# Kernel optimization log

Measured on AMD Instinct MI355X. Metric: run time of the kernel, lower is better.

Reference implementation:

```python
import jax, jax.numpy as jnp
import numpy as np

DIM = 1024
LATENT = 512
HEADS = 16
HEAD_DIM = DIM // HEADS


def setup_inputs() -> dict:
    key = jax.random.key(0)
    ks = jax.random.split(key, 9)
    s = 0.02
    return {
        "x": jax.random.normal(ks[0], (2, 2048, DIM), dtype=jnp.float32),
        "Wq": jax.random.normal(ks[1], (DIM, DIM), dtype=jnp.float32) * s,
        "Wkv": jax.random.normal(ks[2], (DIM, 2 * DIM), dtype=jnp.float32) * s,
        "Wk1": jax.random.normal(ks[3], (DIM, LATENT), dtype=jnp.float32) * s,
        "Wk2": jax.random.normal(ks[4], (LATENT, DIM), dtype=jnp.float32) * s,
        "Wv1": jax.random.normal(ks[5], (DIM, LATENT), dtype=jnp.float32) * s,
        "Wv2": jax.random.normal(ks[6], (LATENT, DIM), dtype=jnp.float32) * s,
        "Wo": jax.random.normal(ks[7], (DIM, DIM), dtype=jnp.float32) * s,
        "bo": jax.random.normal(ks[8], (DIM,), dtype=jnp.float32) * s,
    }


def reference(x, Wq, Wkv, Wk1, Wk2, Wv1, Wv2, Wo, bo):
    b, n, dim = x.shape
    scale = HEAD_DIM ** -0.5
    q = x @ Wq                               # [b, n, dim]
    kv = x @ Wkv                             # [b, n, 2*dim]
    k, v = kv[..., :dim], kv[..., dim:]
    # latent bottleneck MLPs (Linear -> ReLU -> Linear, no bias)
    k = jax.nn.relu(k @ Wk1) @ Wk2           # [b, n, dim]
    v = jax.nn.relu(v @ Wv1) @ Wv2           # [b, n, dim]
    # split heads: [b, n, h*d] -> [b, h, n, d]
    def split_heads(t):
        return t.reshape(b, n, HEADS, HEAD_DIM).transpose(0, 2, 1, 3)
    q = split_heads(q) * scale
    k = split_heads(k)
    v = split_heads(v)
    scores = jnp.einsum('bhid,bhjd->bhij', q, k)   # [b, h, n, n]
    attn = jax.nn.softmax(scores, axis=-1)
    out = jnp.einsum('bhij,bhjd->bhid', attn, v)   # [b, h, n, d]
    out = out.transpose(0, 2, 1, 3).reshape(b, n, dim)
    return out @ Wo + bo
```

## Files before the change

### kernel.cpp

```cpp
#include <hip/hip_runtime.h>
#include <stdint.h>


typedef __attribute__((ext_vector_type(8))) __bf16 bf16x8;
typedef __attribute__((ext_vector_type(4))) float f32x4;

__device__ inline unsigned short f2bfu(float f) {
    __bf16 b = (__bf16)f;
    return __builtin_bit_cast(unsigned short, b);
}

__device__ inline float exp2_fast(float f) {
    return __builtin_amdgcn_exp2f(f);
}

__device__ inline void load_lds16(const void* g, void* l) {
    __builtin_amdgcn_global_load_lds(
        (const __attribute__((address_space(1))) uint32_t*)g,
        (__attribute__((address_space(3))) uint32_t*)l, 16, 0, 0);
}

__device__ inline f32x4 mfma_bf16(bf16x8 a, bf16x8 b, f32x4 c) {
    return __builtin_amdgcn_mfma_f32_16x16x32_bf16(a, b, c, 0, 0, 0);
}


__global__ __launch_bounds__(256) void cvt_x_kernel(
    const float* __restrict__ src, unsigned short* __restrict__ dst)
{
    int i = (blockIdx.x * 256 + threadIdx.x) * 4;
    float4 v = *(const float4*)&src[i];
    ushort4 o;
    o.x = f2bfu(v.x); o.y = f2bfu(v.y); o.z = f2bfu(v.z); o.w = f2bfu(v.w);
    *(ushort4*)&dst[i] = o;
}

__global__ __launch_bounds__(256) void transpose_w2_kernel(
    const float* __restrict__ s0, const float* __restrict__ s1,
    unsigned short* __restrict__ d0, unsigned short* __restrict__ d1,
    int R, int C, float sc0, float sc1)
{
    const float* src = blockIdx.z ? s1 : s0;
    unsigned short* dst = blockIdx.z ? d1 : d0;
    float sc = blockIdx.z ? sc1 : sc0;
    __shared__ float tile[64][65];
    int c0 = blockIdx.x * 64, r0 = blockIdx.y * 64;
    int t = threadIdx.x;
    int col = t & 63, rr = t >> 6;
#pragma unroll
    for (int i = 0; i < 16; ++i)
        tile[rr + i * 4][col] = src[(size_t)(r0 + rr + i * 4) * C + c0 + col];
    __syncthreads();
#pragma unroll
    for (int i = 0; i < 16; ++i) {
        int r2 = rr + i * 4;
        dst[(size_t)(c0 + r2) * R + r0 + col] = f2bfu(tile[col][r2] * sc);
    }
}

__global__ __launch_bounds__(256) void transpose_v_kernel(
    const unsigned short* __restrict__ v, int ldv, unsigned short* __restrict__ vt)
{
    __shared__ unsigned short tile[64][65];
    int n0 = blockIdx.x * 64, bh = blockIdx.y;
    int b = bh >> 4, h = bh & 15;
    int t = threadIdx.x;
    int r = t >> 3, c = t & 7;
#pragma unroll
    for (int p = 0; p < 2; ++p) {
        int row = r + p * 32;
        const unsigned short* src = v + (size_t)(b * 2048 + n0 + row) * ldv + h * 64 + c * 8;
        ushort4 a = *(const ushort4*)src;
        ushort4 b4 = *(const ushort4*)(src + 4);
        tile[row][c * 8 + 0] = a.x;  tile[row][c * 8 + 1] = a.y;
        tile[row][c * 8 + 2] = a.z;  tile[row][c * 8 + 3] = a.w;
        tile[row][c * 8 + 4] = b4.x; tile[row][c * 8 + 5] = b4.y;
        tile[row][c * 8 + 6] = b4.z; tile[row][c * 8 + 7] = b4.w;
    }
    __syncthreads();
#pragma unroll
    for (int p = 0; p < 2; ++p) {
        int d = r + p * 32;
        ushort4 o0, o1;
        o0.x = tile[c * 8 + 0][d]; o0.y = tile[c * 8 + 1][d];
        o0.z = tile[c * 8 + 2][d]; o0.w = tile[c * 8 + 3][d];
        o1.x = tile[c * 8 + 4][d]; o1.y = tile[c * 8 + 5][d];
        o1.z = tile[c * 8 + 6][d]; o1.w = tile[c * 8 + 7][d];
        unsigned short* dp = vt + (size_t)(bh * 64 + d) * 2048 + n0 + c * 8;
        *(ushort4*)dp = o0;
        *(ushort4*)(dp + 4) = o1;
    }
}

template<int BN>
__global__ __launch_bounds__(256) void gemm_bf16_kernel(
    const unsigned short* __restrict__ A0, const unsigned short* __restrict__ A1,
    const unsigned short* __restrict__ B0, const unsigned short* __restrict__ B1,
    void* __restrict__ C0, void* __restrict__ C1,
    int lda, int ldb, int ldc, int K,
    const float* __restrict__ bias, int relu, int out_f32)
{
    const unsigned short* A = blockIdx.z ? A1 : A0;
    const unsigned short* Bt = blockIdx.z ? B1 : B0;
    void* C = blockIdx.z ? C1 : C0;

    constexpr int NI = BN / 32;
    __shared__ unsigned short Als[128 * 32];
    __shared__ unsigned short Bls[BN * 32];
    int t = threadIdx.x;
    int lane = t & 63, w = t >> 6;
    int n0 = blockIdx.x * BN, m0 = blockIdx.y * 128;
    int wm = (w & 1) * 64, wn = (w >> 1) * (BN / 2);
    int lrow = lane & 15, quad = lane >> 4;

    f32x4 acc[4][NI];
    f32x4 z = {0.f, 0.f, 0.f, 0.f};
#pragma unroll
    for (int i = 0; i < 4; ++i)
#pragma unroll
        for (int j = 0; j < NI; ++j) acc[i][j] = z;

    int c0 = t, c1 = t + 256;
    const unsigned short* ag0 = A + (size_t)(m0 + (c0 >> 2)) * lda + (c0 & 3) * 8;
    const unsigned short* ag1 = A + (size_t)(m0 + (c1 >> 2)) * lda + (c1 & 3) * 8;
    const unsigned short* bg0 = Bt + (size_t)(n0 + (c0 >> 2)) * ldb + (c0 & 3) * 8;
    const unsigned short* bg1 = Bt + (size_t)(n0 + ((c1 >> 2) & (BN - 1))) * ldb + (c1 & 3) * 8;

    for (int k0 = 0; k0 < K; k0 += 32) {
        __syncthreads();
        load_lds16(ag0 + k0, &Als[c0 * 8]);
        load_lds16(ag1 + k0, &Als[c1 * 8]);
        load_lds16(bg0 + k0, &Bls[c0 * 8]);
        if constexpr (BN == 128) load_lds16(bg1 + k0, &Bls[c1 * 8]);
        __syncthreads();

        bf16x8 af[4], bfr[NI];
#pragma unroll
        for (int mi = 0; mi < 4; ++mi)
            af[mi] = *(const bf16x8*)&Als[(wm + mi * 16 + lrow) * 32 + quad * 8];
#pragma unroll
        for (int ni = 0; ni < NI; ++ni)
            bfr[ni] = *(const bf16x8*)&Bls[(wn + ni * 16 + lrow) * 32 + quad * 8];
#pragma unroll
        for (int mi = 0; mi < 4; ++mi)
#pragma unroll
            for (int ni = 0; ni < NI; ++ni)
                acc[mi][ni] = mfma_bf16(af[mi], bfr[ni], acc[mi][ni]);
    }

#pragma unroll
    for (int mi = 0; mi < 4; ++mi)
#pragma unroll
        for (int ni = 0; ni < NI; ++ni)
#pragma unroll
            for (int r = 0; r < 4; ++r) {
                int row = m0 + wm + mi * 16 + quad * 4 + r;
                int col = n0 + wn + ni * 16 + lrow;
                float v = acc[mi][ni][r];
                if (bias) v += bias[col];
                if (relu) v = fmaxf(v, 0.0f);
                if (out_f32) ((float*)C)[(size_t)row * ldc + col] = v;
                else ((unsigned short*)C)[(size_t)row * ldc + col] = f2bfu(v);
            }
}

__global__ __launch_bounds__(256, 2) void flash_mfma_kernel(
    const unsigned short* __restrict__ Q, int ldq,
    const unsigned short* __restrict__ K, int ldk,
    const unsigned short* __restrict__ Vt, unsigned short* __restrict__ O)
{
    __shared__ __align__(16) unsigned short Kls[2][2 * 64 * 32];
    __shared__ __align__(16) unsigned short Vls[2][2 * 64 * 32];
    __shared__ __align__(16) unsigned short Pls[4][2][16 * 64];

    int pbid = blockIdx.x;
    int lbid = (pbid >> 3) + (pbid & 7) * 64;
    int q0 = (lbid & 15) * 128, bh = lbid >> 4;
    int b = bh >> 4, h = bh & 15;
    int t = threadIdx.x;
    int lane = t & 63, w = t >> 6;
    int lrow = lane & 15, quad = lane >> 4;

    bf16x8 qf[2][2];
#pragma unroll
    for (int qb = 0; qb < 2; ++qb) {
        const unsigned short* qrow =
            Q + (size_t)(b * 2048 + q0 + w * 32 + qb * 16 + lrow) * ldq + h * 64;
        qf[qb][0] = *(const bf16x8*)&qrow[quad * 8];
        qf[qb][1] = *(const bf16x8*)&qrow[32 + quad * 8];
    }

    f32x4 z = {0.f, 0.f, 0.f, 0.f};
    f32x4 acco[2][4];
    float m_run[2][4], l_run[2][4];
#pragma unroll
    for (int qb = 0; qb < 2; ++qb)
#pragma unroll
        for (int r = 0; r < 4; ++r) {
            acco[qb][r] = z;
            m_run[qb][r] = -1e30f;
            l_run[qb][r] = 0.f;
        }

    int row4 = t >> 2;
    int seg = (t & 3) * 8;
    const unsigned short* kg = K + (size_t)(b * 2048 + row4) * ldk + h * 64 + seg;
    const unsigned short* vg = Vt + (size_t)(bh * 64 + row4) * 2048 + seg;

    char* pb[2] = { (char*)&Pls[w][0][0], (char*)&Pls[w][1][0] };

    load_lds16(kg,      &Kls[0][t * 8]);
    load_lds16(kg + 32, &Kls[0][2048 + t * 8]);
    load_lds16(vg,      &Vls[0][t * 8]);
    load_lds16(vg + 32, &Vls[0][2048 + t * 8]);
    __syncthreads();

    int cur = 0;
    for (int kt = 0; kt < 2048; kt += 64) {
        if (kt + 64 < 2048) {
            const unsigned short* kgk = kg + (size_t)(kt + 64) * ldk;
            const unsigned short* vgk = vg + kt + 64;
            int nb = cur ^ 1;
            load_lds16(kgk,      &Kls[nb][t * 8]);
            load_lds16(kgk + 32, &Kls[nb][2048 + t * 8]);
            load_lds16(vgk,      &Vls[nb][t * 8]);
            load_lds16(vgk + 32, &Vls[nb][2048 + t * 8]);
        }

        f32x4 s[2][4];
        __builtin_amdgcn_s_setprio(1);
#pragma unroll
        for (int kt8 = 0; kt8 < 4; ++kt8) {
            bf16x8 k0 = *(const bf16x8*)&Kls[cur][(kt8 * 16 + lrow) * 32 + quad * 8];
            bf16x8 k1 = *(const bf16x8*)&Kls[cur][2048 + (kt8 * 16 + lrow) * 32 + quad * 8];
            s[0][kt8] = mfma_bf16(qf[0][0], k0, z);
            s[0][kt8] = mfma_bf16(qf[0][1], k1, s[0][kt8]);
            s[1][kt8] = mfma_bf16(qf[1][0], k0, z);
            s[1][kt8] = mfma_bf16(qf[1][1], k1, s[1][kt8]);
        }
        __builtin_amdgcn_s_setprio(0);

#pragma unroll
        for (int qb = 0; qb < 2; ++qb) {
            float pm[4];
#pragma unroll
            for (int r = 0; r < 4; ++r)
                pm[r] = fmaxf(fmaxf(s[qb][0][r], s[qb][1][r]),
                              fmaxf(s[qb][2][r], s[qb][3][r]));
            bool ok = (pm[0] <= m_run[qb][0] + 8.f) && (pm[1] <= m_run[qb][1] + 8.f)
                   && (pm[2] <= m_run[qb][2] + 8.f) && (pm[3] <= m_run[qb][3] + 8.f);
            if (!__all(ok)) {
#pragma unroll
                for (int r = 0; r < 4; ++r) {
#pragma unroll
                    for (int off = 1; off < 16; off <<= 1)
                        pm[r] = fmaxf(pm[r], __shfl_xor(pm[r], off, 64));
                    float mnew = fmaxf(m_run[qb][r], pm[r]);
                    float al = exp2_fast(m_run[qb][r] - mnew);
                    m_run[qb][r] = mnew;
                    l_run[qb][r] *= al;
#pragma unroll
                    for (int nt = 0; nt < 4; ++nt) acco[qb][nt][r] *= al;
                }
            }
#pragma unroll
            for (int kt8 = 0; kt8 < 4; ++kt8)
#pragma unroll
                for (int r = 0; r < 4; ++r) {
                    float p = exp2_fast(s[qb][kt8][r] - m_run[qb][r]);
                    l_run[qb][r] += p;
                    int row = quad * 4 + r;
                    int boff = (row * 128 + (kt8 * 16 + lrow) * 2) ^ ((row & 7) << 4);
                    *(unsigned short*)(pb[qb] + boff) = f2bfu(p);
                }
        }

        __builtin_amdgcn_s_setprio(1);
#pragma unroll
        for (int ks = 0; ks < 2; ++ks) {
            int rb = (lrow * 128 + ks * 64 + quad * 16) ^ ((lrow & 7) << 4);
            bf16x8 pf0 = *(const bf16x8*)(pb[0] + rb);
            bf16x8 pf1 = *(const bf16x8*)(pb[1] + rb);
#pragma unroll
            for (int nt = 0; nt < 4; ++nt) {
                bf16x8 vf = *(const bf16x8*)&Vls[cur][ks * 2048 + (nt * 16 + lrow) * 32 + quad * 8];
                acco[0][nt] = mfma_bf16(pf0, vf, acco[0][nt]);
                acco[1][nt] = mfma_bf16(pf1, vf, acco[1][nt]);
            }
        }
        __builtin_amdgcn_s_setprio(0);

        __syncthreads();
        cur ^= 1;
    }

#pragma unroll
    for (int qb = 0; qb < 2; ++qb)
#pragma unroll
        for (int r = 0; r < 4; ++r) {
            float lr = l_run[qb][r];
#pragma unroll
            for (int off = 1; off < 16; off <<= 1)
                lr += __shfl_xor(lr, off, 64);
            float rl = 1.0f / lr;
            int row = b * 2048 + q0 + w * 32 + qb * 16 + quad * 4 + r;
#pragma unroll
            for (int nt = 0; nt < 4; ++nt)
                O[(size_t)row * 1024 + h * 64 + nt * 16 + lrow] =
                    f2bfu(acco[qb][nt][r] * rl);
        }
}


extern "C" void kernel_launch(void* const* d_in, const int* in_sizes, int n_in,
                              void* d_out, int out_size, void* d_ws, size_t ws_size,
                              hipStream_t stream) {
    const float* x   = (const float*)d_in[0];
    const float* Wq  = (const float*)d_in[1];
    const float* Wkv = (const float*)d_in[2];
    const float* Wk1 = (const float*)d_in[3];
    const float* Wk2 = (const float*)d_in[4];
    const float* Wv1 = (const float*)d_in[5];
    const float* Wv2 = (const float*)d_in[6];
    const float* Wo  = (const float*)d_in[7];
    const float* bo  = (const float*)d_in[8];
    float* out = (float*)d_out;

    unsigned short* p = (unsigned short*)d_ws;
    unsigned short* xb    = p; p += 4194304;
    unsigned short* WqkvT = p; p += 3145728;
    unsigned short* WoT   = p; p += 1048576;
    unsigned short* Wk1T  = p; p += 524288;
    unsigned short* Wv1T  = p; p += 524288;
    unsigned short* Wk2T  = p; p += 524288;
    unsigned short* Wv2T  = p; p += 524288;
    unsigned short* qkv   = p; p += 12582912;
    unsigned short* tmpb  = p; p += 4194304;
    unsigned short* kvo   = p; p += 8388608;
    unsigned short* vtb   = p; p += 4194304;
    unsigned short* attnb = tmpb;

    dim3 blk(256);
    const float qscale = 0.125f * 1.44269504f;

    cvt_x_kernel<<<4096, blk, 0, stream>>>(x, xb);
    transpose_w2_kernel<<<dim3(16, 16, 2), blk, 0, stream>>>(Wq, Wo, WqkvT, WoT, 1024, 1024, qscale, 1.0f);
    transpose_w2_kernel<<<dim3(32, 16, 1), blk, 0, stream>>>(Wkv, Wkv, WqkvT + 1048576, WqkvT + 1048576, 1024, 2048, 1.0f, 1.0f);
    transpose_w2_kernel<<<dim3(8, 16, 2),  blk, 0, stream>>>(Wk1, Wv1, Wk1T, Wv1T, 1024, 512, 1.0f, 1.0f);
    transpose_w2_kernel<<<dim3(16, 8, 2),  blk, 0, stream>>>(Wk2, Wv2, Wk2T, Wv2T, 512, 1024, 1.0f, 1.0f);

    gemm_bf16_kernel<128><<<dim3(24, 32, 1), blk, 0, stream>>>(
        xb, xb, WqkvT, WqkvT, qkv, qkv, 1024, 1024, 3072, 1024, nullptr, 0, 0);
    gemm_bf16_kernel<64><<<dim3(8, 32, 2), blk, 0, stream>>>(
        qkv + 1024, qkv + 2048, Wk1T, Wv1T, tmpb, tmpb + 512,
        3072, 1024, 1024, 1024, nullptr, 1, 0);
    gemm_bf16_kernel<128><<<dim3(8, 32, 2), blk, 0, stream>>>(
        tmpb, tmpb + 512, Wk2T, Wv2T, kvo, kvo + 1024,
        1024, 512, 2048, 512, nullptr, 0, 0);

    transpose_v_kernel<<<dim3(32, 32), blk, 0, stream>>>(kvo + 1024, 2048, vtb);
    flash_mfma_kernel<<<dim3(512), blk, 0, stream>>>(qkv, 3072, kvo, 2048, vtb, attnb);
    gemm_bf16_kernel<64><<<dim3(16, 32, 1), blk, 0, stream>>>(
        attnb, attnb, WoT, WoT, out, out, 1024, 1024, 1024, 1024, bo, 0, 1);
}
```

Baseline: 290.1 us.

## Merge prep kernels into one launch and write transposed V from GEMM epilogue

Folds the x conversion and all weight transpose launches into one prep kernel that dispatches on block index. The V-projection GEMM epilogue now writes V directly in the per-head transposed layout the attention kernel expects. This removes the separate V transpose kernel and its extra read and write of V. K is stored with a narrower leading dimension. The trade-off is several fewer kernel launches against transposed-V stores that are strided rather than row-contiguous.

```diff
diff --git a/kernel.cpp b/kernel.cpp
--- a/kernel.cpp
+++ b/kernel.cpp
@@ -24,75 +24,63 @@
     return __builtin_amdgcn_mfma_f32_16x16x32_bf16(a, b, c, 0, 0, 0);
 }
 
-
-__global__ __launch_bounds__(256) void cvt_x_kernel(
-    const float* __restrict__ src, unsigned short* __restrict__ dst)
+__global__ __launch_bounds__(256) void prep_kernel(
+    const float* __restrict__ x, unsigned short* __restrict__ xb,
+    const float* __restrict__ Wq,  const float* __restrict__ Wo,
+    const float* __restrict__ Wkv,
+    const float* __restrict__ Wk1, const float* __restrict__ Wv1,
+    const float* __restrict__ Wk2, const float* __restrict__ Wv2,
+    unsigned short* __restrict__ WqkvT, unsigned short* __restrict__ WoT,
+    unsigned short* __restrict__ Wk1T,  unsigned short* __restrict__ Wv1T,
+    unsigned short* __restrict__ Wk2T,  unsigned short* __restrict__ Wv2T,
+    float qscale)
 {
-    int i = (blockIdx.x * 256 + threadIdx.x) * 4;
-    float4 v = *(const float4*)&src[i];
-    ushort4 o;
-    o.x = f2bfu(v.x); o.y = f2bfu(v.y); o.z = f2bfu(v.z); o.w = f2bfu(v.w);
-    *(ushort4*)&dst[i] = o;
-}
-
-__global__ __launch_bounds__(256) void transpose_w2_kernel(
-    const float* __restrict__ s0, const float* __restrict__ s1,
-    unsigned short* __restrict__ d0, unsigned short* __restrict__ d1,
-    int R, int C, float sc0, float sc1)
-{
-    const float* src = blockIdx.z ? s1 : s0;
-    unsigned short* dst = blockIdx.z ? d1 : d0;
-    float sc = blockIdx.z ? sc1 : sc0;
     __shared__ float tile[64][65];
-    int c0 = blockIdx.x * 64, r0 = blockIdx.y * 64;
+    int id = blockIdx.x;
     int t = threadIdx.x;
-    int col = t & 63, rr = t >> 6;
+
+    if (id < 4096) {
+        int i = (id * 256 + t) * 4;
+        float4 v = *(const float4*)&x[i];
+        ushort4 o;
+        o.x = f2bfu(v.x); o.y = f2bfu(v.y); o.z = f2bfu(v.z); o.w = f2bfu(v.w);
+        *(ushort4*)&xb[i] = o;
+        return;
+    }
+
+    int r = id - 4096;
+    const float* src; unsigned short* dst; int R, C; float sc; int bx, by;
+    if (r < 512) {
+        int z = r >> 8; int rr = r & 255; bx = rr & 15; by = rr >> 4;
+        src = z ? Wo : Wq; dst = z ? WoT : WqkvT;
+        R = 1024; C = 1024; sc = z ? 1.0f : qscale;
+    } else if (r < 1024) {
+        int rr = r - 512; bx = rr & 31; by = rr >> 5;
+        src = Wkv; dst = WqkvT + 1048576; R = 1024; C = 2048; sc = 1.0f;
+    } else if (r < 1280) {
+        int rr = r - 1024; int z = rr >> 7; rr &= 127; bx = rr & 7; by = rr >> 3;
+        src = z ? Wv1 : Wk1; dst = z ? Wv1T : Wk1T;
+        R = 1024; C = 512; sc = 1.0f;
+    } else {
+        int rr = r - 1280; int z = rr >> 7; rr &= 127; bx = rr & 15; by = rr >> 4;
+        src = z ? Wv2 : Wk2; dst = z ? Wv2T : Wk2T;
+        R = 512; C = 1024; sc = 1.0f;
+    }
+
+    int c0 = bx * 64, r0 = by * 64;
+    int col = t & 63, rr4 = t >> 6;
 #pragma unroll
     for (int i = 0; i < 16; ++i)
-        tile[rr + i * 4][col] = src[(size_t)(r0 + rr + i * 4) * C + c0 + col];
+        tile[rr4 + i * 4][col] = src[(size_t)(r0 + rr4 + i * 4) * C + c0 + col];
     __syncthreads();
 #pragma unroll
     for (int i = 0; i < 16; ++i) {
-        int r2 = rr + i * 4;
+        int r2 = rr4 + i * 4;
         dst[(size_t)(c0 + r2) * R + r0 + col] = f2bfu(tile[col][r2] * sc);
     }
 }
 
-__global__ __launch_bounds__(256) void transpose_v_kernel(
-    const unsigned short* __restrict__ v, int ldv, unsigned short* __restrict__ vt)
-{
-    __shared__ unsigned short tile[64][65];
-    int n0 = blockIdx.x * 64, bh = blockIdx.y;
-    int b = bh >> 4, h = bh & 15;
-    int t = threadIdx.x;
-    int r = t >> 3, c = t & 7;
-#pragma unroll
-    for (int p = 0; p < 2; ++p) {
-        int row = r + p * 32;
-        const unsigned short* src = v + (size_t)(b * 2048 + n0 + row) * ldv + h * 64 + c * 8;
-        ushort4 a = *(const ushort4*)src;
-        ushort4 b4 = *(const ushort4*)(src + 4);
-        tile[row][c * 8 + 0] = a.x;  tile[row][c * 8 + 1] = a.y;
-        tile[row][c * 8 + 2] = a.z;  tile[row][c * 8 + 3] = a.w;
-        tile[row][c * 8 + 4] = b4.x; tile[row][c * 8 + 5] = b4.y;
-        tile[row][c * 8 + 6] = b4.z; tile[row][c * 8 + 7] = b4.w;
-    }
-    __syncthreads();
-#pragma unroll
-    for (int p = 0; p < 2; ++p) {
-        int d = r + p * 32;
-        ushort4 o0, o1;
-        o0.x = tile[c * 8 + 0][d]; o0.y = tile[c * 8 + 1][d];
-        o0.z = tile[c * 8 + 2][d]; o0.w = tile[c * 8 + 3][d];
-        o1.x = tile[c * 8 + 4][d]; o1.y = tile[c * 8 + 5][d];
-        o1.z = tile[c * 8 + 6][d]; o1.w = tile[c * 8 + 7][d];
-        unsigned short* dp = vt + (size_t)(bh * 64 + d) * 2048 + n0 + c * 8;
-        *(ushort4*)dp = o0;
-        *(ushort4*)(dp + 4) = o1;
-    }
-}
-
-template<int BN>
+template<int BN, bool OUTVT = false>
 __global__ __launch_bounds__(256) void gemm_bf16_kernel(
     const unsigned short* __restrict__ A0, const unsigned short* __restrict__ A1,
     const unsigned short* __restrict__ B0, const unsigned short* __restrict__ B1,
@@ -146,6 +134,26 @@
 #pragma unroll
             for (int ni = 0; ni < NI; ++ni)
                 acc[mi][ni] = mfma_bf16(af[mi], bfr[ni], acc[mi][ni]);
+    }
+
+    if (OUTVT && blockIdx.z) {
+        int bb = m0 >> 11;
+        int npb = (m0 & 2047) + wm;
+        unsigned short* vt = (unsigned short*)C;
+#pragma unroll
+        for (int mi = 0; mi < 4; ++mi)
+#pragma unroll
+            for (int ni = 0; ni < NI; ++ni) {
+                int col = n0 + wn + ni * 16 + lrow;
+                int np = npb + mi * 16 + quad * 4;
+                ushort4 o;
+                o.x = f2bfu(acc[mi][ni][0]);
+                o.y = f2bfu(acc[mi][ni][1]);
+                o.z = f2bfu(acc[mi][ni][2]);
+                o.w = f2bfu(acc[mi][ni][3]);
+                *(ushort4*)&vt[(size_t)(bb * 1024 + col) * 2048 + np] = o;
+            }
+        return;
     }
 
 #pragma unroll
@@ -343,23 +351,20 @@
     dim3 blk(256);
     const float qscale = 0.125f * 1.44269504f;
 
-    cvt_x_kernel<<<4096, blk, 0, stream>>>(x, xb);
-    transpose_w2_kernel<<<dim3(16, 16, 2), blk, 0, stream>>>(Wq, Wo, WqkvT, WoT, 1024, 1024, qscale, 1.0f);
-    transpose_w2_kernel<<<dim3(32, 16, 1), blk, 0, stream>>>(Wkv, Wkv, WqkvT + 1048576, WqkvT + 1048576, 1024, 2048, 1.0f, 1.0f);
-    transpose_w2_kernel<<<dim3(8, 16, 2),  blk, 0, stream>>>(Wk1, Wv1, Wk1T, Wv1T, 1024, 512, 1.0f, 1.0f);
-    transpose_w2_kernel<<<dim3(16, 8, 2),  blk, 0, stream>>>(Wk2, Wv2, Wk2T, Wv2T, 512, 1024, 1.0f, 1.0f);
+    prep_kernel<<<5632, blk, 0, stream>>>(
+        x, xb, Wq, Wo, Wkv, Wk1, Wv1, Wk2, Wv2,
+        WqkvT, WoT, Wk1T, Wv1T, Wk2T, Wv2T, qscale);
 
     gemm_bf16_kernel<128><<<dim3(24, 32, 1), blk, 0, stream>>>(
         xb, xb, WqkvT, WqkvT, qkv, qkv, 1024, 1024, 3072, 1024, nullptr, 0, 0);
     gemm_bf16_kernel<64><<<dim3(8, 32, 2), blk, 0, stream>>>(
         qkv + 1024, qkv + 2048, Wk1T, Wv1T, tmpb, tmpb + 512,
         3072, 1024, 1024, 1024, nullptr, 1, 0);
-    gemm_bf16_kernel<128><<<dim3(8, 32, 2), blk, 0, stream>>>(
-        tmpb, tmpb + 512, Wk2T, Wv2T, kvo, kvo + 1024,
-        1024, 512, 2048, 512, nullptr, 0, 0);
-
-    transpose_v_kernel<<<dim3(32, 32), blk, 0, stream>>>(kvo + 1024, 2048, vtb);
-    flash_mfma_kernel<<<dim3(512), blk, 0, stream>>>(qkv, 3072, kvo, 2048, vtb, attnb);
+    gemm_bf16_kernel<128, true><<<dim3(8, 32, 2), blk, 0, stream>>>(
+        tmpb, tmpb + 512, Wk2T, Wv2T, kvo, vtb,
+        1024, 512, 1024, 512, nullptr, 0, 0);
+
+    flash_mfma_kernel<<<dim3(512), blk, 0, stream>>>(qkv, 3072, kvo, 1024, vtb, attnb);
     gemm_bf16_kernel<64><<<dim3(16, 32, 1), blk, 0, stream>>>(
         attnb, attnb, WoT, WoT, out, out, 1024, 1024, 1024, 1024, bo, 0, 1);
 }
```

New measurement: 281.3 us. 3.1% less time.
